# Kernel optimization log

Measured on AMD Instinct MI355X. Metric: run time of the kernel, lower is better.

Reference implementation:

```python
import jax, jax.numpy as jnp
import numpy as np

N, E = 50000, 400000
HID, HT = 128, 128
HEADS, C = 4, 128  # TransformerConv heads=4, out_channels=hidden_X


def setup_inputs() -> dict:
    key = jax.random.key(0)
    ks = jax.random.split(key, 16)
    s = lambda k, shape, fan: jax.random.normal(k, shape, jnp.float32) / np.sqrt(fan)
    return {
        "edge_index": jax.random.randint(ks[0], (2, E), 0, N, dtype=jnp.int32),
        "h_X": jax.random.normal(ks[1], (N, HID), jnp.float32),
        "h_t": jax.random.normal(ks[2], (1, HT), jnp.float32),
        # TransformerConv params: lin_query/key/value: (HID -> HEADS*C), lin_skip: (HID -> C)
        "Wq": s(ks[3], (HID, HEADS * C), HID), "bq": jnp.zeros((HEADS * C,), jnp.float32),
        "Wk": s(ks[4], (HID, HEADS * C), HID), "bk": jnp.zeros((HEADS * C,), jnp.float32),
        "Wv": s(ks[5], (HID, HEADS * C), HID), "bv": jnp.zeros((HEADS * C,), jnp.float32),
        "Wskip": s(ks[6], (HID, C), HID), "bskip": jnp.zeros((C,), jnp.float32),
        # update_X: Linear(HID+HT -> HID), LayerNorm(HID)
        "Wup": s(ks[7], (HID + HT, HID), HID + HT), "bup": jnp.zeros((HID,), jnp.float32),
        "gamma": jnp.ones((HID,), jnp.float32), "beta": jnp.zeros((HID,), jnp.float32),
    }


def transformer_conv(h_X, edge_index, Wq, bq, Wk, bk, Wv, bv, Wskip, bskip):
    n = h_X.shape[0]
    src, dst = edge_index[0], edge_index[1]  # messages flow src -> dst
    q = (h_X @ Wq + bq).reshape(n, HEADS, C)
    k = (h_X @ Wk + bk).reshape(n, HEADS, C)
    v = (h_X @ Wv + bv).reshape(n, HEADS, C)
    # per-edge attention scores [E, H]
    score = jnp.einsum('ehc,ehc->eh', q[dst], k[src]) / np.sqrt(C)
    # segment softmax over incoming edges of each destination node
    m = jax.ops.segment_max(score, dst, num_segments=n)          # [N, H]
    ex = jnp.exp(score - m[dst])                                 # [E, H]
    denom = jax.ops.segment_sum(ex, dst, num_segments=n)        # [N, H]
    alpha = ex / denom[dst]                                      # [E, H]
    agg = jax.ops.segment_sum(alpha[..., None] * v[src], dst, num_segments=n)  # [N, H, C]
    out = agg.mean(axis=1)                                       # concat=False -> mean over heads
    return out + h_X @ Wskip + bskip                             # root_weight=True


def reference(edge_index, h_X, h_t, Wq, bq, Wk, bk, Wv, bv, Wskip, bskip,
              Wup, bup, gamma, beta):
    n = h_X.shape[0]
    h_att = transformer_conv(h_X, edge_index, Wq, bq, Wk, bk, Wv, bv, Wskip, bskip)
    h_t_exp = jnp.broadcast_to(h_t, (n, h_t.shape[1]))
    h = jnp.concatenate([h_att, h_t_exp], axis=1)
    h = jax.nn.relu(h @ Wup + bup)
    # LayerNorm (eps=1e-5); Dropout is identity in eval
    mu = h.mean(axis=-1, keepdims=True)
    var = ((h - mu) ** 2).mean(axis=-1, keepdims=True)
    return (h - mu) / jnp.sqrt(var + 1e-5) * gamma + beta
```

## Files before the change

### kernel.cpp

```cpp
#include <hip/hip_runtime.h>

typedef unsigned short u16;
typedef unsigned int   u32;

#define HID   128
#define HEADS 4
#define CH    128
#define HC    512
#define UT    32

typedef __bf16 bf16x8v __attribute__((ext_vector_type(8)));
typedef float  f32x4v  __attribute__((ext_vector_type(4)));
union FragU { uint4 u; bf16x8v b; };

static __device__ __forceinline__ float bf2f(u16 u) {
  union { u32 u; float f; } x;
  x.u = ((u32)u) << 16;
  return x.f;
}
static __device__ __forceinline__ u16 f2bf(float f) {
  union { float f; u32 u; } x;
  x.f = f;
  u32 r = x.u + 0x7fffu + ((x.u >> 16) & 1u);
  return (u16)(r >> 16);
}

static __device__ __forceinline__ void unpack8(uint4 raw, float* dst) {
  dst[0] = bf2f((u16)(raw.x & 0xffffu));
  dst[1] = bf2f((u16)(raw.x >> 16));
  dst[2] = bf2f((u16)(raw.y & 0xffffu));
  dst[3] = bf2f((u16)(raw.y >> 16));
  dst[4] = bf2f((u16)(raw.z & 0xffffu));
  dst[5] = bf2f((u16)(raw.z >> 16));
  dst[6] = bf2f((u16)(raw.w & 0xffffu));
  dst[7] = bf2f((u16)(raw.w >> 16));
}

static __device__ __forceinline__ void gld_lds16(const u16* g, u16* l) {
  __builtin_amdgcn_global_load_lds(
      (__attribute__((address_space(1))) const void*)g,
      (__attribute__((address_space(3))) void*)l, 16, 0, 0);
}

__global__ void zero_kernel(int* p, int n) {
  int i = blockIdx.x * 256 + threadIdx.x;
  if (i < n) p[i] = 0;
}

__global__ void hist_kernel(const int* dst_idx, int* deg, int E) {
  int e = blockIdx.x * 256 + threadIdx.x;
  if (e < E) atomicAdd(&deg[dst_idx[e]], 1);
}

__global__ void blocksum_kernel(const int* deg, int* bsums, int n) {
  __shared__ int buf[256];
  int i = blockIdx.x * 256 + threadIdx.x;
  int v = 0;
  if (i < n) v = deg[i];
  buf[threadIdx.x] = v;
  __syncthreads();
  for (int off = 128; off > 0; off >>= 1) {
    if (threadIdx.x < off) buf[threadIdx.x] += buf[threadIdx.x + off];
    __syncthreads();
  }
  if (threadIdx.x == 0) bsums[blockIdx.x] = buf[0];
}

__global__ void scanb_kernel(const int* bsums, int* boffs, int nb) {
  __shared__ int buf[256];
  __shared__ int carry_s;
  int tid = threadIdx.x;
  if (tid == 0) carry_s = 0;
  __syncthreads();
  for (int base = 0; base < nb; base += 256) {
    int i = base + tid;
    int v = 0;
    if (i < nb) v = bsums[i];
    buf[tid] = v;
    __syncthreads();
    for (int off = 1; off < 256; off <<= 1) {
      int t = 0;
      if (tid >= off) t = buf[tid - off];
      __syncthreads();
      buf[tid] += t;
      __syncthreads();
    }
    int incl = buf[tid] + carry_s;
    if (i < nb) boffs[i] = incl - v;
    __syncthreads();
    if (tid == 255) carry_s = incl;
    __syncthreads();
  }
}

__global__ void scanfinal_kernel(const int* deg, const int* boffs,
                                 int* row_ptr, int* cursor, int n) {
  __shared__ int buf[256];
  int tid = threadIdx.x;
  int i = blockIdx.x * 256 + tid;
  int v = 0;
  if (i < n) v = deg[i];
  buf[tid] = v;
  __syncthreads();
  for (int off = 1; off < 256; off <<= 1) {
    int t = 0;
    if (tid >= off) t = buf[tid - off];
    __syncthreads();
    buf[tid] += t;
    __syncthreads();
  }
  int incl = buf[tid] + boffs[blockIdx.x];
  if (i < n) {
    row_ptr[i + 1] = incl;
    cursor[i] = incl - v;
  }
  if (i == 0) row_ptr[0] = 0;
}

__global__ void scatter_kernel(const int* src_idx, const int* dst_idx,
                               int* cursor, int* col, int E) {
  int e = blockIdx.x * 256 + threadIdx.x;
  if (e < E) {
    int pos = atomicAdd(&cursor[dst_idx[e]], 1);
    col[pos] = src_idx[e];
  }
}

__global__ void packH_kernel(const float* __restrict__ hX,
                             u16* __restrict__ hpack, int N, int total) {
  int i = blockIdx.x * 256 + threadIdx.x;
  if (i >= total) return;
  int j = i & 7;
  int lane = (i >> 3) & 63;
  int kc = (i >> 9) & 3;
  int ntile = i >> 11;
  int node = ntile * 16 + (lane & 15);
  int k = kc * 32 + (lane >> 4) * 8 + j;
  float v = (node < N) ? hX[(size_t)node * HID + k] : 0.f;
  hpack[i] = f2bf(v);
}

__global__ void packW4_kernel(const float* __restrict__ Wq,
                              const float* __restrict__ Wk,
                              const float* __restrict__ Wv,
                              const float* __restrict__ Wsk,
                              u16* __restrict__ Wp, int total) {
  int i = blockIdx.x * 256 + threadIdx.x;
  if (i >= total) return;
  int j = i & 7;
  int lane = (i >> 3) & 63;
  int kc = (i >> 9) & 3;
  int ct = i >> 11;
  int n = ct * 16 + (lane & 15);
  int k = kc * 32 + (lane >> 4) * 8 + j;
  float w;
  if (n < 512) w = Wq[(size_t)k * HC + n];
  else if (n < 1024) w = Wk[(size_t)k * HC + (n - 512)];
  else if (n < 1536) w = Wv[(size_t)k * HC + (n - 1024)];
  else w = Wsk[(size_t)k * HID + (n - 1536)];
  Wp[i] = f2bf(w);
}

__global__ __launch_bounds__(256) void mfma_proj_kernel(
    const u16* __restrict__ hpack, const u16* __restrict__ Wp,
    const float* __restrict__ bq, const float* __restrict__ bk,
    const float* __restrict__ bv, const float* __restrict__ bsk,
    u16* __restrict__ qb, u16* __restrict__ kbuf, u16* __restrict__ vbuf,
    float* __restrict__ skipf, int N) {
  __shared__ u16 Al[8 * 2048];
  __shared__ u16 Bl[8 * 2048];
  int t = threadIdx.x;
  int wv = t >> 6;
  int L = t & 63;
  int bx = blockIdx.x;
  int my = blockIdx.y;

  const u16* srcA = hpack + (size_t)my * (8 * 2048);
  const u16* srcB = Wp + (size_t)bx * (8 * 2048);
  int ldso = (t & 192) * 8;
#pragma unroll
  for (int it = 0; it < 8; ++it) {
    gld_lds16(srcA + it * 2048 + t * 8, Al + it * 2048 + ldso);
    gld_lds16(srcB + it * 2048 + t * 8, Bl + it * 2048 + ldso);
  }
  __syncthreads();

  f32x4v acc[8][2];
#pragma unroll
  for (int mt = 0; mt < 8; ++mt) {
    acc[mt][0] = (f32x4v){0.f, 0.f, 0.f, 0.f};
    acc[mt][1] = (f32x4v){0.f, 0.f, 0.f, 0.f};
  }

#pragma unroll
  for (int kc = 0; kc < 4; ++kc) {
    FragU b0, b1;
    b0.u = *(const uint4*)(Bl + (2 * wv) * 2048 + kc * 512 + L * 8);
    b1.u = *(const uint4*)(Bl + (2 * wv + 1) * 2048 + kc * 512 + L * 8);
#pragma unroll
    for (int mt = 0; mt < 8; ++mt) {
      FragU a;
      a.u = *(const uint4*)(Al + mt * 2048 + kc * 512 + L * 8);
      acc[mt][0] =
          __builtin_amdgcn_mfma_f32_16x16x32_bf16(a.b, b0.b, acc[mt][0], 0, 0, 0);
      acc[mt][1] =
          __builtin_amdgcn_mfma_f32_16x16x32_bf16(a.b, b1.b, acc[mt][1], 0, 0, 0);
    }
  }

  int colq = L & 15;
  int quad = L >> 4;
#pragma unroll
  for (int cc = 0; cc < 2; ++cc) {
    int ct = bx * 8 + 2 * wv + cc;
    int n = ct * 16 + colq;
    u16* outB;
    const float* bias;
    int nl;
    int isF32 = 0;
    if (n < 512) {
      outB = qb; bias = bq; nl = n;
    } else if (n < 1024) {
      outB = kbuf; bias = bk; nl = n - 512;
    } else if (n < 1536) {
      outB = vbuf; bias = bv; nl = n - 1024;
    } else {
      outB = (u16*)skipf; bias = bsk; nl = n - 1536; isF32 = 1;
    }
    float bval = bias[nl];
#pragma unroll
    for (int mt = 0; mt < 8; ++mt) {
#pragma unroll
      for (int rg = 0; rg < 4; ++rg) {
        int node = (my * 8 + mt) * 16 + quad * 4 + rg;
        if (node < N) {
          float val = acc[mt][cc][rg] + bval;
          if (isF32) {
            skipf[(size_t)node * HID + nl] = val;
          } else {
            outB[(size_t)node * HC + nl] = f2bf(val);
          }
        }
      }
    }
  }
}

__global__ void fused_attn_kernel(const u16* __restrict__ qb,
                                  const u16* __restrict__ kb,
                                  const u16* __restrict__ vb,
                                  const int* __restrict__ row_ptr,
                                  const int* __restrict__ col_src,
                                  float* out, int N) {
  int node = blockIdx.x * 4 + (threadIdx.x >> 6);
  if (node >= N) return;
  int lane = threadIdx.x & 63;
  int head = lane >> 4;
  int r = lane & 15;
  int foff = head * CH + r * 8;
  const float sscale = 0.08838834764831845f;

  float qf[8];
  unpack8(*(const uint4*)(qb + (size_t)node * HC + foff), qf);

  float m = -3.402823466e38f;
  float l = 0.f;
  float acc[8];
  for (int j = 0; j < 8; ++j) acc[j] = 0.f;

  int e0 = row_ptr[node];
  int e1 = row_ptr[node + 1];
  int e = e0;

  for (; e + 4 <= e1; e += 4) {
    int s0 = col_src[e];
    int s1 = col_src[e + 1];
    int s2 = col_src[e + 2];
    int s3 = col_src[e + 3];
    uint4 k0 = *(const uint4*)(kb + (size_t)s0 * HC + foff);
    uint4 k1 = *(const uint4*)(kb + (size_t)s1 * HC + foff);
    uint4 k2 = *(const uint4*)(kb + (size_t)s2 * HC + foff);
    uint4 k3 = *(const uint4*)(kb + (size_t)s3 * HC + foff);
    uint4 v0 = *(const uint4*)(vb + (size_t)s0 * HC + foff);
    uint4 v1 = *(const uint4*)(vb + (size_t)s1 * HC + foff);
    uint4 v2 = *(const uint4*)(vb + (size_t)s2 * HC + foff);
    uint4 v3 = *(const uint4*)(vb + (size_t)s3 * HC + foff);

    float kf0[8], kf1[8], kf2[8], kf3[8];
    unpack8(k0, kf0);
    unpack8(k1, kf1);
    unpack8(k2, kf2);
    unpack8(k3, kf3);
    float p0 = 0.f, p1 = 0.f, p2 = 0.f, p3 = 0.f;
    for (int j = 0; j < 8; ++j) {
      p0 = fmaf(kf0[j], qf[j], p0);
      p1 = fmaf(kf1[j], qf[j], p1);
      p2 = fmaf(kf2[j], qf[j], p2);
      p3 = fmaf(kf3[j], qf[j], p3);
    }
    p0 += __shfl_xor(p0, 1);
    p1 += __shfl_xor(p1, 1);
    p2 += __shfl_xor(p2, 1);
    p3 += __shfl_xor(p3, 1);
    p0 += __shfl_xor(p0, 2);
    p1 += __shfl_xor(p1, 2);
    p2 += __shfl_xor(p2, 2);
    p3 += __shfl_xor(p3, 2);
    p0 += __shfl_xor(p0, 4);
    p1 += __shfl_xor(p1, 4);
    p2 += __shfl_xor(p2, 4);
    p3 += __shfl_xor(p3, 4);
    p0 += __shfl_xor(p0, 8);
    p1 += __shfl_xor(p1, 8);
    p2 += __shfl_xor(p2, 8);
    p3 += __shfl_xor(p3, 8);
    float sc0 = p0 * sscale;
    float sc1 = p1 * sscale;
    float sc2 = p2 * sscale;
    float sc3 = p3 * sscale;
    float mnew = fmaxf(fmaxf(m, fmaxf(sc0, sc1)), fmaxf(sc2, sc3));
    float so = __expf(m - mnew);
    float pe0 = __expf(sc0 - mnew);
    float pe1 = __expf(sc1 - mnew);
    float pe2 = __expf(sc2 - mnew);
    float pe3 = __expf(sc3 - mnew);
    l = l * so + (pe0 + pe1) + (pe2 + pe3);
    float vf0[8], vf1[8], vf2[8], vf3[8];
    unpack8(v0, vf0);
    unpack8(v1, vf1);
    unpack8(v2, vf2);
    unpack8(v3, vf3);
    for (int j = 0; j < 8; ++j) {
      float add = fmaf(pe0, vf0[j],
                       fmaf(pe1, vf1[j], fmaf(pe2, vf2[j], pe3 * vf3[j])));
      acc[j] = fmaf(acc[j], so, add);
    }
    m = mnew;
  }

  for (; e < e1; ++e) {
    int s0 = col_src[e];
    uint4 k0 = *(const uint4*)(kb + (size_t)s0 * HC + foff);
    uint4 v0 = *(const uint4*)(vb + (size_t)s0 * HC + foff);
    float kf0[8];
    unpack8(k0, kf0);
    float p0 = 0.f;
    for (int j = 0; j < 8; ++j) p0 = fmaf(kf0[j], qf[j], p0);
    p0 += __shfl_xor(p0, 1);
    p0 += __shfl_xor(p0, 2);
    p0 += __shfl_xor(p0, 4);
    p0 += __shfl_xor(p0, 8);
    float sc0 = p0 * sscale;
    float mnew = fmaxf(m, sc0);
    float so = __expf(m - mnew);
    float pe0 = __expf(sc0 - mnew);
    l = l * so + pe0;
    float vf0[8];
    unpack8(v0, vf0);
    for (int j = 0; j < 8; ++j) acc[j] = fmaf(acc[j], so, pe0 * vf0[j]);
    m = mnew;
  }

  float inv = 0.f;
  if (l > 0.f) inv = 1.0f / l;
  float val[8];
  for (int j = 0; j < 8; ++j) {
    float x = acc[j] * inv;
    x += __shfl_xor(x, 16);
    x += __shfl_xor(x, 32);
    val[j] = x * 0.25f;
  }

  if (head == 0) {
    float* p = out + (size_t)node * HID + r * 8;
    float4 a = *(const float4*)(p);
    float4 b = *(const float4*)(p + 4);
    a.x += val[0]; a.y += val[1]; a.z += val[2]; a.w += val[3];
    b.x += val[4]; b.y += val[5]; b.z += val[6]; b.w += val[7];
    *(float4*)(p) = a;
    *(float4*)(p + 4) = b;
  }
}

__global__ void cvec_kernel(const float* h_t, const float* Wup,
                            const float* bup, float* cvec) {
  __shared__ float part[4][128];
  int c = threadIdx.x & 127;
  int kc = threadIdx.x >> 7;
  float acc = 0.f;
  for (int k = kc * 32; k < kc * 32 + 32; ++k)
    acc = fmaf(h_t[k], Wup[(size_t)(128 + k) * 128 + c], acc);
  part[kc][c] = acc;
  __syncthreads();
  if (kc == 0)
    cvec[c] = part[0][c] + part[1][c] + part[2][c] + part[3][c] + bup[c];
}

__global__ __launch_bounds__(256) void ATTLayer_19396072308956_kernel(
    float* out, const float* __restrict__ Wup, const float* __restrict__ cvec,
    const float* __restrict__ gamma, const float* __restrict__ beta, int N) {
  __shared__ float Wl[64 * 128];
  __shared__ float Hl[UT * 128];
  int t = threadIdx.x;
  int n0 = blockIdx.x * UT;

  for (int i = t * 4; i < UT * 128; i += 1024) {
    int node = n0 + (i >> 7);
    float4 v;
    if (node < N) {
      v = *(const float4*)(out + (size_t)node * HID + (i & 127));
    } else {
      v.x = 0.f; v.y = 0.f; v.z = 0.f; v.w = 0.f;
    }
    *(float4*)(Hl + i) = v;
  }

  int wv = t >> 6;
  int r = t & 63;
  int c0 = 2 * r;
  float2 cv = *(const float2*)(cvec + c0);
  float a0[8];
  float a1[8];
  for (int j = 0; j < 8; ++j) {
    a0[j] = cv.x;
    a1[j] = cv.y;
  }

  for (int ph = 0; ph < 2; ++ph) {
    __syncthreads();
    for (int i = t * 4; i < 64 * 128; i += 1024) {
      *(float4*)(Wl + i) = *(const float4*)(Wup + (size_t)ph * 64 * 128 + i);
    }
    __syncthreads();
    const float* hbase = Hl + (wv * 8) * 128 + ph * 64;
#pragma unroll 8
    for (int k = 0; k < 64; ++k) {
      float2 w2 = *(const float2*)(Wl + k * 128 + c0);
      for (int j = 0; j < 8; ++j) {
        float h = hbase[j * 128 + k];
        a0[j] = fmaf(h, w2.x, a0[j]);
        a1[j] = fmaf(h, w2.y, a1[j]);
      }
    }
  }

  float2 g = *(const float2*)(gamma + c0);
  float2 b = *(const float2*)(beta + c0);
  for (int j = 0; j < 8; ++j) {
    int node = n0 + wv * 8 + j;
    float r0 = fmaxf(a0[j], 0.f);
    float r1 = fmaxf(a1[j], 0.f);
    float s = r0 + r1;
    for (int msk = 1; msk < 64; msk <<= 1) s += __shfl_xor(s, msk);
    float mean = s * (1.0f / 128.0f);
    float d0 = r0 - mean;
    float d1 = r1 - mean;
    float sq = d0 * d0 + d1 * d1;
    for (int msk = 1; msk < 64; msk <<= 1) sq += __shfl_xor(sq, msk);
    float rstd = rsqrtf(sq * (1.0f / 128.0f) + 1e-5f);
    if (node < N) {
      float2 o;
      o.x = d0 * rstd * g.x + b.x;
      o.y = d1 * rstd * g.y + b.y;
      *(float2*)(out + (size_t)node * HID + c0) = o;
    }
  }
}

extern "C" void kernel_launch(void* const* d_in, const int* in_sizes, int n_in,
                              void* d_out, int out_size, void* d_ws,
                              size_t ws_size, hipStream_t stream) {
  (void)n_in;
  (void)out_size;
  (void)ws_size;

  const int* edge_index = (const int*)d_in[0];
  const float* hX    = (const float*)d_in[1];
  const float* h_t   = (const float*)d_in[2];
  const float* Wq    = (const float*)d_in[3];
  const float* bq    = (const float*)d_in[4];
  const float* Wk    = (const float*)d_in[5];
  const float* bk    = (const float*)d_in[6];
  const float* Wv    = (const float*)d_in[7];
  const float* bv    = (const float*)d_in[8];
  const float* Wskip = (const float*)d_in[9];
  const float* bskip = (const float*)d_in[10];
  const float* Wup   = (const float*)d_in[11];
  const float* bup   = (const float*)d_in[12];
  const float* gamma = (const float*)d_in[13];
  const float* beta  = (const float*)d_in[14];

  const int E = in_sizes[0] / 2;
  const int N = in_sizes[1] / HID;
  const int* src_idx = edge_index;
  const int* dst_idx = edge_index + E;
  const int NB = (N + 255) / 256;
  const int NTILES = (N + 15) / 16;
  const int NTILES8 = ((NTILES + 7) / 8) * 8;

  char* w = (char*)d_ws;
  size_t off = 0;
  float* cvec = (float*)(w + off);
  off += 256 * 4;
  int* deg = (int*)(w + off);
  off += ((size_t)N * 4 + 255) / 256 * 256;
  int* row_ptr = (int*)(w + off);
  off += ((size_t)(N + 1) * 4 + 255) / 256 * 256;
  int* cursor = (int*)(w + off);
  off += ((size_t)N * 4 + 255) / 256 * 256;
  int* bsums = (int*)(w + off);
  off += ((size_t)NB * 4 + 255) / 256 * 256;
  int* boffs = (int*)(w + off);
  off += ((size_t)NB * 4 + 255) / 256 * 256;
  int* col = (int*)(w + off);
  off += ((size_t)E * 4 + 255) / 256 * 256;
  u16* hpack = (u16*)(w + off);
  off += ((size_t)NTILES8 * 2048 * 2 + 255) / 256 * 256;
  u16* Wp = (u16*)(w + off);
  off += ((size_t)128 * 1664 * 2 + 255) / 256 * 256;
  u16* bigA = (u16*)(w + off);
  off += ((size_t)N * HC * 2 + 255) / 256 * 256;
  u16* bigB = (u16*)(w + off);
  off += ((size_t)N * HC * 2 + 255) / 256 * 256;
  u16* bigC = (u16*)(w + off);
  off += ((size_t)N * HC * 2 + 255) / 256 * 256;

  float* out = (float*)d_out;

  zero_kernel<<<NB, 256, 0, stream>>>(deg, N);
  hist_kernel<<<(E + 255) / 256, 256, 0, stream>>>(dst_idx, deg, E);
  blocksum_kernel<<<NB, 256, 0, stream>>>(deg, bsums, N);
  scanb_kernel<<<1, 256, 0, stream>>>(bsums, boffs, NB);
  scanfinal_kernel<<<NB, 256, 0, stream>>>(deg, boffs, row_ptr, cursor, N);
  scatter_kernel<<<(E + 255) / 256, 256, 0, stream>>>(src_idx, dst_idx, cursor,
                                                      col, E);

  int totH = NTILES8 * 2048;
  packH_kernel<<<(totH + 255) / 256, 256, 0, stream>>>(hX, hpack, N, totH);
  packW4_kernel<<<(128 * 1664 + 255) / 256, 256, 0, stream>>>(
      Wq, Wk, Wv, Wskip, Wp, 128 * 1664);

  cvec_kernel<<<1, 512, 0, stream>>>(h_t, Wup, bup, cvec);

  mfma_proj_kernel<<<dim3(13, NTILES8 / 8), 256, 0, stream>>>(
      hpack, Wp, bq, bk, bv, bskip, bigA, bigB, bigC, out, N);

  fused_attn_kernel<<<(N + 3) / 4, 256, 0, stream>>>(bigA, bigB, bigC, row_ptr,
                                                     col, out, N);

  ATTLayer_19396072308956_kernel<<<(N + UT - 1) / UT, 256, 0, stream>>>(
      out, Wup, cvec, gamma, beta, N);
}
```

Before: 456.9 us.

## Drop LDS staging in projection GEMM; hold B fragments in registers

```diff
diff --git a/kernel.cpp b/kernel.cpp
--- a/kernel.cpp
+++ b/kernel.cpp
@@ -34,12 +34,6 @@
   dst[5] = bf2f((u16)(raw.z >> 16));
   dst[6] = bf2f((u16)(raw.w & 0xffffu));
   dst[7] = bf2f((u16)(raw.w >> 16));
-}
-
-static __device__ __forceinline__ void gld_lds16(const u16* g, u16* l) {
-  __builtin_amdgcn_global_load_lds(
-      (__attribute__((address_space(1))) const void*)g,
-      (__attribute__((address_space(3))) void*)l, 16, 0, 0);
 }
 
 __global__ void zero_kernel(int* p, int n) {
@@ -167,78 +161,90 @@
     const float* __restrict__ bv, const float* __restrict__ bsk,
     u16* __restrict__ qb, u16* __restrict__ kbuf, u16* __restrict__ vbuf,
     float* __restrict__ skipf, int N) {
-  __shared__ u16 Al[8 * 2048];
-  __shared__ u16 Bl[8 * 2048];
   int t = threadIdx.x;
   int wv = t >> 6;
   int L = t & 63;
   int bx = blockIdx.x;
-  int my = blockIdx.y;
-
-  const u16* srcA = hpack + (size_t)my * (8 * 2048);
-  const u16* srcB = Wp + (size_t)bx * (8 * 2048);
-  int ldso = (t & 192) * 8;
-#pragma unroll
-  for (int it = 0; it < 8; ++it) {
-    gld_lds16(srcA + it * 2048 + t * 8, Al + it * 2048 + ldso);
-    gld_lds16(srcB + it * 2048 + t * 8, Bl + it * 2048 + ldso);
-  }
-  __syncthreads();
-
-  f32x4v acc[8][2];
-#pragma unroll
-  for (int mt = 0; mt < 8; ++mt) {
-    acc[mt][0] = (f32x4v){0.f, 0.f, 0.f, 0.f};
-    acc[mt][1] = (f32x4v){0.f, 0.f, 0.f, 0.f};
-  }
-
-#pragma unroll
-  for (int kc = 0; kc < 4; ++kc) {
-    FragU b0, b1;
-    b0.u = *(const uint4*)(Bl + (2 * wv) * 2048 + kc * 512 + L * 8);
-    b1.u = *(const uint4*)(Bl + (2 * wv + 1) * 2048 + kc * 512 + L * 8);
-#pragma unroll
-    for (int mt = 0; mt < 8; ++mt) {
-      FragU a;
-      a.u = *(const uint4*)(Al + mt * 2048 + kc * 512 + L * 8);
-      acc[mt][0] =
-          __builtin_amdgcn_mfma_f32_16x16x32_bf16(a.b, b0.b, acc[mt][0], 0, 0, 0);
-      acc[mt][1] =
-          __builtin_amdgcn_mfma_f32_16x16x32_bf16(a.b, b1.b, acc[mt][1], 0, 0, 0);
-    }
-  }
+  int my0 = blockIdx.y * 8;
+
+  FragU Bf[2][4];
+  const u16* wb0 = Wp + (size_t)(bx * 8 + wv * 2) * 2048;
+#pragma unroll
+  for (int cc = 0; cc < 2; ++cc)
+#pragma unroll
+    for (int kc = 0; kc < 4; ++kc)
+      Bf[cc][kc].u = *(const uint4*)(wb0 + cc * 2048 + kc * 512 + L * 8);
 
   int colq = L & 15;
   int quad = L >> 4;
+  u16* outB_[2];
+  float bval[2];
+  int nl_[2];
+  int isF32_[2];
 #pragma unroll
   for (int cc = 0; cc < 2; ++cc) {
-    int ct = bx * 8 + 2 * wv + cc;
-    int n = ct * 16 + colq;
-    u16* outB;
+    int n = (bx * 8 + wv * 2 + cc) * 16 + colq;
     const float* bias;
-    int nl;
-    int isF32 = 0;
     if (n < 512) {
-      outB = qb; bias = bq; nl = n;
+      outB_[cc] = qb; bias = bq; nl_[cc] = n; isF32_[cc] = 0;
     } else if (n < 1024) {
-      outB = kbuf; bias = bk; nl = n - 512;
+      outB_[cc] = kbuf; bias = bk; nl_[cc] = n - 512; isF32_[cc] = 0;
     } else if (n < 1536) {
-      outB = vbuf; bias = bv; nl = n - 1024;
+      outB_[cc] = vbuf; bias = bv; nl_[cc] = n - 1024; isF32_[cc] = 0;
     } else {
-      outB = (u16*)skipf; bias = bsk; nl = n - 1536; isF32 = 1;
-    }
-    float bval = bias[nl];
-#pragma unroll
-    for (int mt = 0; mt < 8; ++mt) {
-#pragma unroll
-      for (int rg = 0; rg < 4; ++rg) {
-        int node = (my * 8 + mt) * 16 + quad * 4 + rg;
-        if (node < N) {
-          float val = acc[mt][cc][rg] + bval;
-          if (isF32) {
-            skipf[(size_t)node * HID + nl] = val;
-          } else {
-            outB[(size_t)node * HC + nl] = f2bf(val);
+      outB_[cc] = (u16*)skipf; bias = bsk; nl_[cc] = n - 1536; isF32_[cc] = 1;
+    }
+    bval[cc] = bias[nl_[cc]];
+  }
+
+  const u16* ha = hpack + (size_t)my0 * 2048;
+
+  for (int mt = 0; mt < 8; mt += 2) {
+    FragU a0[4], a1[4];
+#pragma unroll
+    for (int kc = 0; kc < 4; ++kc) {
+      a0[kc].u = *(const uint4*)(ha + (size_t)mt * 2048 + kc * 512 + L * 8);
+      a1[kc].u =
+          *(const uint4*)(ha + (size_t)(mt + 1) * 2048 + kc * 512 + L * 8);
+    }
+
+    f32x4v ac00 = (f32x4v){0.f, 0.f, 0.f, 0.f};
+    f32x4v ac01 = (f32x4v){0.f, 0.f, 0.f, 0.f};
+    f32x4v ac10 = (f32x4v){0.f, 0.f, 0.f, 0.f};
+    f32x4v ac11 = (f32x4v){0.f, 0.f, 0.f, 0.f};
+#pragma unroll
+    for (int kc = 0; kc < 4; ++kc) {
+      ac00 = __builtin_amdgcn_mfma_f32_16x16x32_bf16(a0[kc].b, Bf[0][kc].b,
+                                                     ac00, 0, 0, 0);
+      ac01 = __builtin_amdgcn_mfma_f32_16x16x32_bf16(a0[kc].b, Bf[1][kc].b,
+                                                     ac01, 0, 0, 0);
+      ac10 = __builtin_amdgcn_mfma_f32_16x16x32_bf16(a1[kc].b, Bf[0][kc].b,
+                                                     ac10, 0, 0, 0);
+      ac11 = __builtin_amdgcn_mfma_f32_16x16x32_bf16(a1[kc].b, Bf[1][kc].b,
+                                                     ac11, 0, 0, 0);
+    }
+
+#pragma unroll
+    for (int half = 0; half < 2; ++half) {
+      int nodeBase = (my0 + mt + half) * 16 + quad * 4;
+#pragma unroll
+      for (int cc = 0; cc < 2; ++cc) {
+        const f32x4v& a =
+            half ? (cc ? ac11 : ac10) : (cc ? ac01 : ac00);
+        if (isF32_[cc]) {
+#pragma unroll
+          for (int rg = 0; rg < 4; ++rg) {
+            int node = nodeBase + rg;
+            if (node < N)
+              skipf[(size_t)node * HID + nl_[cc]] = a[rg] + bval[cc];
+          }
+        } else {
+          u16* ob = outB_[cc];
+#pragma unroll
+          for (int rg = 0; rg < 4; ++rg) {
+            int node = nodeBase + rg;
+            if (node < N)
+              ob[(size_t)node * HC + nl_[cc]] = f2bf(a[rg] + bval[cc]);
           }
         }
       }
```

Measured after the change: 394.5 us. -13.7%, faster.
